# Kernel optimization log

Hardware: AMD Instinct MI355X
Metric: run time of the kernel (lower is better)

Reference implementation:

```python
import jax, jax.numpy as jnp
import numpy as np

B, S, F_IN = 8, 2048, 1024
H, SC = 512, 256
N_LAYERS = 3


def _glorot(key, shape):
    fan_in, fan_out = shape[-2], shape[-1]
    lim = float(np.sqrt(6.0 / (fan_in + fan_out)))
    return jax.random.uniform(key, shape, jnp.float32, -lim, lim)


def setup_inputs() -> dict:
    key = jax.random.key(0)
    ks = jax.random.split(key, 8)
    x = jax.random.normal(ks[0], (B, S, F_IN), jnp.float32)
    Wp = _glorot(ks[1], (F_IN, H)); bp = jnp.zeros((H,), jnp.float32)
    gcn_W = _glorot(ks[2], (N_LAYERS, H, H)); gcn_b = jnp.zeros((N_LAYERS, H), jnp.float32)
    s1_W = _glorot(ks[3], (H, SC)); s1_b = jnp.zeros((SC,), jnp.float32)
    s2_W = _glorot(ks[4], (SC, SC // 2)); s2_b = jnp.zeros((SC // 2,), jnp.float32)
    s3_W = _glorot(ks[5], (SC // 2, 1)); s3_b = jnp.zeros((1,), jnp.float32)
    return {"x": x, "Wp": Wp, "bp": bp, "gcn_W": gcn_W, "gcn_b": gcn_b,
            "s1_W": s1_W, "s1_b": s1_b, "s2_W": s2_W, "s2_b": s2_b,
            "s3_W": s3_W, "s3_b": s3_b}


def _build_adj(seq_len):
    # tridiagonal band: self + immediate temporal neighbors
    a = jnp.eye(seq_len, dtype=jnp.float32)
    a = a + jnp.eye(seq_len, k=1, dtype=jnp.float32) + jnp.eye(seq_len, k=-1, dtype=jnp.float32)
    deg = a.sum(axis=1)
    dinv = jnp.power(deg + 1e-8, -0.5)
    # D^{-1/2} A D^{-1/2}
    return dinv[:, None] * a * dinv[None, :]


def reference(x, Wp, bp, gcn_W, gcn_b, s1_W, s1_b, s2_W, s2_b, s3_W, s3_b):
    seq_len = x.shape[1]
    adj = _build_adj(seq_len)  # [S, S]
    h = jnp.einsum('bsf,fh->bsh', x, Wp) + bp  # feature projection
    for i in range(N_LAYERS):
        support = jnp.einsum('bsh,hk->bsk', h, gcn_W[i])
        h = jnp.einsum('st,btk->bsk', adj, support) + gcn_b[i]
        if i < N_LAYERS - 1:
            h = jax.nn.relu(h)  # dropout is identity in eval mode
    z = jax.nn.relu(jnp.einsum('bsh,hc->bsc', h, s1_W) + s1_b)
    z = jax.nn.relu(jnp.einsum('bsc,cd->bsd', z, s2_W) + s2_b)
    scores = jax.nn.sigmoid(jnp.einsum('bsd,do->bso', z, s3_W) + s3_b)
    return scores[..., 0]  # [B, S]
```

## Files before the change

kernel.cpp:

```cpp
#include <hip/hip_runtime.h>
#include <hip/hip_fp16.h>
#include <cstdint>
#include <cstddef>


typedef _Float16 f16;
typedef _Float16 f16x8 __attribute__((ext_vector_type(8)));
typedef float    f32x4 __attribute__((ext_vector_type(4)));

__device__ __forceinline__ void async_cp16(const void* g, void* l) {
  __builtin_amdgcn_global_load_lds((const __attribute__((address_space(1))) void*)g,
                                   (__attribute__((address_space(3))) void*)l, 16, 0, 0);
}

__device__ __forceinline__ f16x8 splat8(f16 v) {
  f16x8 r;
#pragma unroll
  for (int e = 0; e < 8; ++e) r[e] = v;
  return r;
}

template<int BM, int BN, int WAVES_M, int WAVES_N, bool RELU, bool HAS_BIAS, int AMODE>
__global__ __launch_bounds__(256, 4) void gemm_f16_kernel(
    const void* __restrict__ Aptr, const f16* __restrict__ BT,
    f16* __restrict__ C, const float* __restrict__ bias,
    int M, int N, int K)
{
  constexpr int BK = 64;
  constexpr int WM = BM / WAVES_M;
  constexpr int WN = BN / WAVES_N;
  constexpr int TM = WM / 16;
  constexpr int TN = WN / 16;
  constexpr int ITER_A = (BM * BK) / (256 * 8);
  constexpr int ITER_B = (BN * BK) / (256 * 8);
  constexpr int S = 2048;

  __shared__ __align__(16) f16 sA[BM * BK];
  __shared__ __align__(16) f16 sB[BN * BK];

  const int tid  = threadIdx.x;
  const int lane = tid & 63;
  const int wave = tid >> 6;
  const int wm   = wave / WAVES_N;
  const int wn   = wave % WAVES_N;
  const int m0   = blockIdx.x * BM;
  const int n0   = blockIdx.y * BN;

  uint32_t offA[ITER_A][3];
  f16      cfA[ITER_A][3];
  const float dM = 0.57735026919f;
  const float dE = 0.70710678118f;
#pragma unroll
  for (int j = 0; j < ITER_A; ++j) {
    const int linear = j * 256 + tid;
    const int row = linear >> 3;
    const int q   = (linear & 7) ^ (row & 7);
    const int gm  = m0 + row;
    if constexpr (AMODE == 1) {
      offA[j][0] = (uint32_t)(((size_t)gm * K + q * 8) * 4);
    } else {
      const int s = gm & (S - 1);
      const float dsv = (s == 0 || s == S - 1) ? dE : dM;
      const float cpf = (s > 0)     ? dsv * ((s - 1 == 0) ? dE : dM)     : 0.0f;
      const float csf = dsv * dsv;
      const float cnf = (s < S - 1) ? dsv * ((s + 1 == S - 1) ? dE : dM) : 0.0f;
      const int rm1 = (s > 0)     ? gm - 1 : gm;
      const int rp1 = (s < S - 1) ? gm + 1 : gm;
      offA[j][0] = (uint32_t)(((size_t)rm1 * K + q * 8) * 2);
      offA[j][1] = (uint32_t)(((size_t)gm  * K + q * 8) * 2);
      offA[j][2] = (uint32_t)(((size_t)rp1 * K + q * 8) * 2);
      cfA[j][0] = (f16)cpf; cfA[j][1] = (f16)csf; cfA[j][2] = (f16)cnf;
    }
  }

  f32x4 acc[TM][TN];
#pragma unroll
  for (int i = 0; i < TM; ++i)
#pragma unroll
    for (int j = 0; j < TN; ++j)
      acc[i][j] = (f32x4){0.f, 0.f, 0.f, 0.f};

  const int quad = lane >> 4;
  const int l16  = lane & 15;

  for (int kt = 0; kt < K; kt += BK) {
    __syncthreads();
    if constexpr (AMODE == 1) {
      const char* base = (const char*)Aptr + (size_t)kt * 4;
#pragma unroll
      for (int j = 0; j < ITER_A; ++j) {
        const float4* p = (const float4*)(base + offA[j][0]);
        const float4 a = p[0], b = p[1];
        f16x8 o;
        o[0] = (f16)a.x;  o[1] = (f16)a.y;  o[2] = (f16)a.z;  o[3] = (f16)a.w;
        o[4] = (f16)b.x;  o[5] = (f16)b.y;  o[6] = (f16)b.z;  o[7] = (f16)b.w;
        *(f16x8*)&sA[(size_t)(j * 256 + tid) * 8] = o;
      }
    } else {
      const char* base = (const char*)Aptr + (size_t)kt * 2;
#pragma unroll
      for (int j = 0; j < ITER_A; ++j) {
        f16x8 pv = *(const f16x8*)(base + offA[j][0]);
        f16x8 sv = *(const f16x8*)(base + offA[j][1]);
        f16x8 nv = *(const f16x8*)(base + offA[j][2]);
        f16x8 r = pv * splat8(cfA[j][0]);
        r += sv * splat8(cfA[j][1]);
        r += nv * splat8(cfA[j][2]);
        *(f16x8*)&sA[(size_t)(j * 256 + tid) * 8] = r;
      }
    }
#pragma unroll
    for (int j = 0; j < ITER_B; ++j) {
      const int linear = j * 256 + tid;
      const int row = linear >> 3;
      const int q   = (linear & 7) ^ (row & 7);
      async_cp16(BT + (size_t)(n0 + row) * K + kt + q * 8, &sB[linear * 8]);
    }
    __syncthreads();

#pragma unroll
    for (int kk = 0; kk < 2; ++kk) {
      const int c = quad + kk * 4;
      f16x8 af[TM], bf[TN];
#pragma unroll
      for (int mi = 0; mi < TM; ++mi) {
        const int ml = wm * WM + mi * 16 + l16;
        af[mi] = *(const f16x8*)&sA[ml * 64 + ((c ^ (ml & 7)) * 8)];
      }
#pragma unroll
      for (int ni = 0; ni < TN; ++ni) {
        const int nl = wn * WN + ni * 16 + l16;
        bf[ni] = *(const f16x8*)&sB[nl * 64 + ((c ^ (nl & 7)) * 8)];
      }
#pragma unroll
      for (int mi = 0; mi < TM; ++mi)
#pragma unroll
        for (int ni = 0; ni < TN; ++ni)
          acc[mi][ni] = __builtin_amdgcn_mfma_f32_16x16x32_f16(
              af[mi], bf[ni], acc[mi][ni], 0, 0, 0);
    }
  }

#pragma unroll
  for (int ni = 0; ni < TN; ++ni) {
    const int nc = n0 + wn * WN + ni * 16 + l16;
    const float bv = HAS_BIAS ? bias[nc] : 0.0f;
#pragma unroll
    for (int mi = 0; mi < TM; ++mi) {
#pragma unroll
      for (int r = 0; r < 4; ++r) {
        const int mr = m0 + wm * WM + mi * 16 + quad * 4 + r;
        float v = acc[mi][ni][r] + bv;
        if (RELU) v = fmaxf(v, 0.0f);
        C[(size_t)mr * N + nc] = (f16)v;
      }
    }
  }
}

__global__ __launch_bounds__(256) void head_fused_kernel(
    const f16* __restrict__ h, const f16* __restrict__ S1T,
    const f16* __restrict__ S2T,
    const float* __restrict__ s1b, const float* __restrict__ s2b,
    const float* __restrict__ s3w, const float* __restrict__ s3b,
    float* __restrict__ out)
{
  __shared__ __align__(16) char smem[36864 + 32 * 264 * 2];
  f16* sA  = (f16*)smem;
  f16* sB  = (f16*)(smem + 4096);
  f16* zs  = (f16*)(smem + 36864);
  f16* z2s = (f16*)smem;
  f16* sB2 = (f16*)(smem + 8704);

  const int tid  = threadIdx.x;
  const int lane = tid & 63;
  const int wave = tid >> 6;
  const int quad = lane >> 4;
  const int l16  = lane & 15;
  const int m0   = blockIdx.x * 32;

  f32x4 acc[2][4];
#pragma unroll
  for (int i = 0; i < 2; ++i)
#pragma unroll
    for (int j = 0; j < 4; ++j) acc[i][j] = (f32x4){0.f, 0.f, 0.f, 0.f};

  for (int kt = 0; kt < 512; kt += 64) {
    __syncthreads();
    {
      const int linear = tid;
      const int row = linear >> 3;
      const int q   = (linear & 7) ^ (row & 7);
      async_cp16(h + (size_t)(m0 + row) * 512 + kt + q * 8, &sA[linear * 8]);
    }
#pragma unroll
    for (int j = 0; j < 8; ++j) {
      const int linear = j * 256 + tid;
      const int row = linear >> 3;
      const int q   = (linear & 7) ^ (row & 7);
      async_cp16(S1T + (size_t)row * 512 + kt + q * 8, &sB[linear * 8]);
    }
    __syncthreads();
#pragma unroll
    for (int kk = 0; kk < 2; ++kk) {
      const int c = quad + kk * 4;
      f16x8 af[2], bf[4];
#pragma unroll
      for (int mi = 0; mi < 2; ++mi) {
        const int ml = mi * 16 + l16;
        af[mi] = *(const f16x8*)&sA[ml * 64 + ((c ^ (ml & 7)) * 8)];
      }
#pragma unroll
      for (int ni = 0; ni < 4; ++ni) {
        const int nl = wave * 64 + ni * 16 + l16;
        bf[ni] = *(const f16x8*)&sB[nl * 64 + ((c ^ (nl & 7)) * 8)];
      }
#pragma unroll
      for (int mi = 0; mi < 2; ++mi)
#pragma unroll
        for (int ni = 0; ni < 4; ++ni)
          acc[mi][ni] = __builtin_amdgcn_mfma_f32_16x16x32_f16(
              af[mi], bf[ni], acc[mi][ni], 0, 0, 0);
    }
  }
#pragma unroll
  for (int ni = 0; ni < 4; ++ni) {
    const int nc = wave * 64 + ni * 16 + l16;
    const float bv = s1b[nc];
#pragma unroll
    for (int mi = 0; mi < 2; ++mi)
#pragma unroll
      for (int r = 0; r < 4; ++r) {
        const int row = mi * 16 + quad * 4 + r;
        zs[row * 264 + nc] = (f16)fmaxf(acc[mi][ni][r] + bv, 0.0f);
      }
  }
  __syncthreads();

  f32x4 acc2[2][2];
#pragma unroll
  for (int i = 0; i < 2; ++i)
#pragma unroll
    for (int j = 0; j < 2; ++j) acc2[i][j] = (f32x4){0.f, 0.f, 0.f, 0.f};

  for (int kt2 = 0; kt2 < 4; ++kt2) {
    __syncthreads();
#pragma unroll
    for (int j = 0; j < 4; ++j) {
      const int linear = j * 256 + tid;
      const int row = linear >> 3;
      const int q   = (linear & 7) ^ (row & 7);
      async_cp16(S2T + (size_t)row * 256 + kt2 * 64 + q * 8, &sB2[linear * 8]);
    }
    __syncthreads();
#pragma unroll
    for (int kk = 0; kk < 2; ++kk) {
      const int c = quad + kk * 4;
      f16x8 af[2], bf[2];
#pragma unroll
      for (int mi = 0; mi < 2; ++mi) {
        const int row = mi * 16 + l16;
        af[mi] = *(const f16x8*)&zs[row * 264 + (kt2 * 8 + c) * 8];
      }
#pragma unroll
      for (int ni = 0; ni < 2; ++ni) {
        const int nl = wave * 32 + ni * 16 + l16;
        bf[ni] = *(const f16x8*)&sB2[nl * 64 + ((c ^ (nl & 7)) * 8)];
      }
#pragma unroll
      for (int mi = 0; mi < 2; ++mi)
#pragma unroll
        for (int ni = 0; ni < 2; ++ni)
          acc2[mi][ni] = __builtin_amdgcn_mfma_f32_16x16x32_f16(
              af[mi], bf[ni], acc2[mi][ni], 0, 0, 0);
    }
  }
  __syncthreads();
#pragma unroll
  for (int ni = 0; ni < 2; ++ni) {
    const int nc = wave * 32 + ni * 16 + l16;
    const float bv = s2b[nc];
#pragma unroll
    for (int mi = 0; mi < 2; ++mi)
#pragma unroll
      for (int r = 0; r < 4; ++r) {
        const int row = mi * 16 + quad * 4 + r;
        z2s[row * 136 + nc] = (f16)fmaxf(acc2[mi][ni][r] + bv, 0.0f);
      }
  }
  __syncthreads();

  const int m  = tid >> 3;
  const int qd = tid & 7;
  float p = 0.f;
#pragma unroll
  for (int j = 0; j < 2; ++j) {
    f16x8 v = *(const f16x8*)&z2s[m * 136 + qd * 16 + j * 8];
#pragma unroll
    for (int e = 0; e < 8; ++e) p += (float)v[e] * s3w[qd * 16 + j * 8 + e];
  }
  p += __shfl_xor(p, 1);
  p += __shfl_xor(p, 2);
  p += __shfl_xor(p, 4);
  if (qd == 0) out[m0 + m] = 1.0f / (1.0f + expf(-(p + s3b[0])));
}

__global__ __launch_bounds__(256) void prep_kernel(
    const float* __restrict__ Wp, f16* __restrict__ WpT,
    const float* __restrict__ gW, f16* __restrict__ GT,
    const float* __restrict__ s1W, f16* __restrict__ S1T,
    const float* __restrict__ s2W, f16* __restrict__ S2T)
{
  __shared__ f16 s[64 * 68];
  const int tid = threadIdx.x;
  int b = blockIdx.x;

  const float* W; f16* WT; int K, N, tile;
  if (b < 128)      { W = Wp;  WT = WpT; K = 1024; N = 512; tile = b; }
  else if (b < 320) { const int i = (b - 128) >> 6;
                      W = gW + (size_t)i * 262144; WT = GT + (size_t)i * 262144;
                      K = 512; N = 512; tile = (b - 128) & 63; }
  else if (b < 352) { W = s1W; WT = S1T; K = 512; N = 256; tile = b - 320; }
  else              { W = s2W; WT = S2T; K = 256; N = 128; tile = b - 352; }

  const int nt = tile % (N >> 6);
  const int kt = tile / (N >> 6);
#pragma unroll
  for (int it = 0; it < 16; ++it) {
    const int i  = it * 256 + tid;
    const int rk = i >> 6, rn = i & 63;
    s[rn * 68 + rk] = (f16)W[(size_t)(kt * 64 + rk) * N + nt * 64 + rn];
  }
  __syncthreads();
#pragma unroll
  for (int it = 0; it < 16; ++it) {
    const int i  = it * 256 + tid;
    const int rn = i >> 6, rk = i & 63;
    WT[(size_t)(nt * 64 + rn) * K + kt * 64 + rk] = s[rn * 68 + rk];
  }
}

extern "C" void kernel_launch(void* const* d_in, const int* in_sizes, int n_in,
                              void* d_out, int out_size, void* d_ws, size_t ws_size,
                              hipStream_t stream) {
  (void)in_sizes; (void)n_in; (void)out_size; (void)ws_size;
  const float* x   = (const float*)d_in[0];
  const float* Wp  = (const float*)d_in[1];
  const float* bp  = (const float*)d_in[2];
  const float* gW  = (const float*)d_in[3];
  const float* gb  = (const float*)d_in[4];
  const float* s1W = (const float*)d_in[5];
  const float* s1b = (const float*)d_in[6];
  const float* s2W = (const float*)d_in[7];
  const float* s2b = (const float*)d_in[8];
  const float* s3W = (const float*)d_in[9];
  const float* s3b = (const float*)d_in[10];
  float* out = (float*)d_out;

  constexpr int M = 16384;
  char* ws = (char*)d_ws;
  f16* hA  = (f16*)(ws + 0);
  f16* hB  = (f16*)(ws + 16777216);
  f16* WpT = (f16*)(ws + 33554432);
  f16* GT  = (f16*)(ws + 34603008);
  f16* S1T = (f16*)(ws + 36175872);
  f16* S2T = (f16*)(ws + 36438016);

  prep_kernel<<<360, 256, 0, stream>>>(Wp, WpT, gW, GT, s1W, S1T, s2W, S2T);

  gemm_f16_kernel<64, 128, 2, 2, false, true, 1>
      <<<dim3(M / 64, 4), 256, 0, stream>>>(x, WpT, hA, bp, M, 512, 1024);

  gemm_f16_kernel<64, 128, 2, 2, true, true, 2>
      <<<dim3(M / 64, 4), 256, 0, stream>>>(hA, GT, hB, gb, M, 512, 512);
  gemm_f16_kernel<64, 128, 2, 2, true, true, 2>
      <<<dim3(M / 64, 4), 256, 0, stream>>>(hB, GT + 262144, hA, gb + 512, M, 512, 512);
  gemm_f16_kernel<64, 128, 2, 2, false, true, 2>
      <<<dim3(M / 64, 4), 256, 0, stream>>>(hA, GT + 524288, hB, gb + 1024, M, 512, 512);

  head_fused_kernel<<<M / 32, 256, 0, stream>>>(hB, S1T, S2T, s1b, s2b, s3W, s3b, out);
}
```

Measured before the change: 211.1 us.

## Double-buffer LDS tiles and prefetch next K-tile during MFMA compute

Splits the GEMM main loop into issue/write/compute stages with two LDS buffers for A and B. The next tile's global loads (async B copies and A register loads) are issued before computing the current tile, and the A tile is written to the other buffer afterwards. This cuts the loop to one barrier per iteration and hides global memory latency behind the MFMAs. In exchange it doubles LDS use and holds the prefetched A data in registers, which may lower occupancy under launch_bounds(256,4).

```diff
diff --git a/kernel.cpp b/kernel.cpp
--- a/kernel.cpp
+++ b/kernel.cpp
@@ -35,8 +35,8 @@
   constexpr int ITER_B = (BN * BK) / (256 * 8);
   constexpr int S = 2048;
 
-  __shared__ __align__(16) f16 sA[BM * BK];
-  __shared__ __align__(16) f16 sB[BN * BK];
+  __shared__ __align__(16) f16 sA[2][BM * BK];
+  __shared__ __align__(16) f16 sB[2][BN * BK];
 
   const int tid  = threadIdx.x;
   const int lane = tid & 63;
@@ -83,41 +83,53 @@
   const int quad = lane >> 4;
   const int l16  = lane & 15;
 
-  for (int kt = 0; kt < K; kt += BK) {
-    __syncthreads();
-    if constexpr (AMODE == 1) {
-      const char* base = (const char*)Aptr + (size_t)kt * 4;
-#pragma unroll
-      for (int j = 0; j < ITER_A; ++j) {
-        const float4* p = (const float4*)(base + offA[j][0]);
-        const float4 a = p[0], b = p[1];
-        f16x8 o;
-        o[0] = (f16)a.x;  o[1] = (f16)a.y;  o[2] = (f16)a.z;  o[3] = (f16)a.w;
-        o[4] = (f16)b.x;  o[5] = (f16)b.y;  o[6] = (f16)b.z;  o[7] = (f16)b.w;
-        *(f16x8*)&sA[(size_t)(j * 256 + tid) * 8] = o;
-      }
-    } else {
-      const char* base = (const char*)Aptr + (size_t)kt * 2;
-#pragma unroll
-      for (int j = 0; j < ITER_A; ++j) {
-        f16x8 pv = *(const f16x8*)(base + offA[j][0]);
-        f16x8 sv = *(const f16x8*)(base + offA[j][1]);
-        f16x8 nv = *(const f16x8*)(base + offA[j][2]);
-        f16x8 r = pv * splat8(cfA[j][0]);
-        r += sv * splat8(cfA[j][1]);
-        r += nv * splat8(cfA[j][2]);
-        *(f16x8*)&sA[(size_t)(j * 256 + tid) * 8] = r;
-      }
-    }
+  float4 pa[ITER_A][2];
+  f16x8  pv[ITER_A], sv[ITER_A], nv[ITER_A];
+
+  auto stageB_issue = [&](int kt, int buf) {
 #pragma unroll
     for (int j = 0; j < ITER_B; ++j) {
       const int linear = j * 256 + tid;
       const int row = linear >> 3;
       const int q   = (linear & 7) ^ (row & 7);
-      async_cp16(BT + (size_t)(n0 + row) * K + kt + q * 8, &sB[linear * 8]);
-    }
-    __syncthreads();
-
+      async_cp16(BT + (size_t)(n0 + row) * K + kt + q * 8, &sB[buf][linear * 8]);
+    }
+  };
+  auto stageA_issue = [&](int kt) {
+    if constexpr (AMODE == 1) {
+      const char* base = (const char*)Aptr + (size_t)kt * 4;
+#pragma unroll
+      for (int j = 0; j < ITER_A; ++j) {
+        const float4* p = (const float4*)(base + offA[j][0]);
+        pa[j][0] = p[0]; pa[j][1] = p[1];
+      }
+    } else {
+      const char* base = (const char*)Aptr + (size_t)kt * 2;
+#pragma unroll
+      for (int j = 0; j < ITER_A; ++j) {
+        pv[j] = *(const f16x8*)(base + offA[j][0]);
+        sv[j] = *(const f16x8*)(base + offA[j][1]);
+        nv[j] = *(const f16x8*)(base + offA[j][2]);
+      }
+    }
+  };
+  auto stageA_write = [&](int buf) {
+#pragma unroll
+    for (int j = 0; j < ITER_A; ++j) {
+      f16x8 o;
+      if constexpr (AMODE == 1) {
+        const float4 a = pa[j][0], b = pa[j][1];
+        o[0] = (f16)a.x;  o[1] = (f16)a.y;  o[2] = (f16)a.z;  o[3] = (f16)a.w;
+        o[4] = (f16)b.x;  o[5] = (f16)b.y;  o[6] = (f16)b.z;  o[7] = (f16)b.w;
+      } else {
+        o  = pv[j] * splat8(cfA[j][0]);
+        o += sv[j] * splat8(cfA[j][1]);
+        o += nv[j] * splat8(cfA[j][2]);
+      }
+      *(f16x8*)&sA[buf][(size_t)(j * 256 + tid) * 8] = o;
+    }
+  };
+  auto compute = [&](int buf) {
 #pragma unroll
     for (int kk = 0; kk < 2; ++kk) {
       const int c = quad + kk * 4;
@@ -125,12 +137,12 @@
 #pragma unroll
       for (int mi = 0; mi < TM; ++mi) {
         const int ml = wm * WM + mi * 16 + l16;
-        af[mi] = *(const f16x8*)&sA[ml * 64 + ((c ^ (ml & 7)) * 8)];
+        af[mi] = *(const f16x8*)&sA[buf][ml * 64 + ((c ^ (ml & 7)) * 8)];
       }
 #pragma unroll
       for (int ni = 0; ni < TN; ++ni) {
         const int nl = wn * WN + ni * 16 + l16;
-        bf[ni] = *(const f16x8*)&sB[nl * 64 + ((c ^ (nl & 7)) * 8)];
+        bf[ni] = *(const f16x8*)&sB[buf][nl * 64 + ((c ^ (nl & 7)) * 8)];
       }
 #pragma unroll
       for (int mi = 0; mi < TM; ++mi)
@@ -139,6 +151,25 @@
           acc[mi][ni] = __builtin_amdgcn_mfma_f32_16x16x32_f16(
               af[mi], bf[ni], acc[mi][ni], 0, 0, 0);
     }
+  };
+
+  stageB_issue(0, 0);
+  stageA_issue(0);
+  stageA_write(0);
+  __syncthreads();
+
+  const int nt = K / BK;
+  int cur = 0;
+  for (int t = 0; t < nt; ++t) {
+    const bool pf = (t + 1 < nt);
+    if (pf) {
+      stageB_issue((t + 1) * BK, cur ^ 1);
+      stageA_issue((t + 1) * BK);
+    }
+    compute(cur);
+    if (pf) stageA_write(cur ^ 1);
+    __syncthreads();
+    cur ^= 1;
   }
 
 #pragma unroll
```

New measurement: 221.7 us. 1.05x slower.
